# Performance work log

Measured on AMD Instinct MI355X. Metric: run time of the kernel, lower is better.

The kernel has to match this reference:

```python
import jax, jax.numpy as jnp
import numpy as np

E = 500_000
N = 30_000
R = 6
H = 256
OE = 256
OUT = 1
L = 3          # num_layers
A = 2          # num_aux + 1 branches


def setup_inputs() -> dict:
    key = jax.random.key(0)
    ks = jax.random.split(key, 9)
    x = jax.random.normal(ks[0], (E, H), dtype=jnp.float32)
    rbf = jax.random.normal(ks[1], (E, R), dtype=jnp.float32)
    i = jax.random.randint(ks[2], (E,), 0, N, dtype=jnp.int64)
    # parameters (stored in [in, out] convention)
    s = 1.0 / np.sqrt(H)
    W_rbf = jax.random.normal(ks[3], (R, H), dtype=jnp.float32) / np.sqrt(R)
    W_up = jax.random.normal(ks[4], (A, H, OE), dtype=jnp.float32) * s
    W_hidden = jax.random.normal(ks[5], (A, L, OE, OE), dtype=jnp.float32) / np.sqrt(OE)
    b_hidden = jnp.zeros((A, L, OE), dtype=jnp.float32)
    W_out = jax.random.normal(ks[6], (A, OE, OUT), dtype=jnp.float32) / np.sqrt(OE)
    return {"x": x, "rbf": rbf, "i": i, "num_nodes": N,
            "W_rbf": W_rbf, "W_up": W_up, "W_hidden": W_hidden,
            "b_hidden": b_hidden, "W_out": W_out}


def reference(x, rbf, i, num_nodes, W_rbf, W_up, W_hidden, b_hidden, W_out):
    # elementwise multiply of per-edge features by radial basis projection,
    # then segment-sum over edge target index -> per-node features [N, H]
    msg = (rbf @ W_rbf) * x                     # [E, H]
    h = jax.ops.segment_sum(msg, i, num_segments=num_nodes)  # [N, H]
    outs = []
    for a in range(A):
        y = h @ W_up[a]                          # [N, OE]
        for l in range(L):
            y = jax.nn.silu(y @ W_hidden[a, l] + b_hidden[a, l])
        outs.append(y @ W_out[a])               # [N, OUT]
    return tuple(outs)
```

## Files before the change

kernel.cpp:

```cpp
#include <hip/hip_runtime.h>

#define E_EDGES 500000
#define N_NODES 30000
#define H_DIM   256

typedef float  floatx4 __attribute__((ext_vector_type(4)));
typedef short  shortx4 __attribute__((ext_vector_type(4)));
typedef short  shortx8 __attribute__((ext_vector_type(8)));
typedef __bf16 bf16x8  __attribute__((ext_vector_type(8)));

__device__ inline short f2bf(float f) {
    unsigned u = __builtin_bit_cast(unsigned, f);
    u += 0x7fffu + ((u >> 16) & 1u);
    return (short)(u >> 16);
}
__device__ inline float bf2f(short s) {
    unsigned u = ((unsigned)(unsigned short)s) << 16;
    return __builtin_bit_cast(float, u);
}

__global__ __launch_bounds__(256) void prep_weights(
    const float* __restrict__ wup, const float* __restrict__ whid,
    short* __restrict__ wfrag)
{
    int g   = blockIdx.x * 256 + threadIdx.x;
    int mat = g >> 13;
    int grp = g & 8191;
    int a = mat >> 2, lay = mat & 3;
    const float* src = (lay == 0) ? (wup + a * 65536)
                                  : (whid + (a * 3 + lay - 1) * 65536);
    int ks  = grp >> 10;
    int rem = grp & 1023;
    int ntg = rem >> 6;
    int lane = rem & 63;
    int q = lane >> 4, c = lane & 15;
    int col = ntg * 16 + c;
    int k0  = ks * 32 + q * 8;
    shortx8 v;
#pragma unroll
    for (int j = 0; j < 8; j++) v[j] = f2bf(src[(k0 + j) * 256 + col]);
    ((shortx8*)wfrag)[g] = v;
}

__global__ __launch_bounds__(256) void hist_kernel(
    const int* __restrict__ idx, int* __restrict__ counts)
{
    int e = blockIdx.x * 256 + threadIdx.x;
    if (e < E_EDGES) atomicAdd(&counts[idx[e]], 1);
}

__global__ __launch_bounds__(1024) void scan_kernel(
    const int* __restrict__ counts, int* __restrict__ offsets,
    int* __restrict__ cursor)
{
    const int t = threadIdx.x;
    const int lane = t & 63, wave = t >> 6;
    const int base = t * 30;
    int local[30];
    int s = 0;
#pragma unroll
    for (int j = 0; j < 30; j++) {
        int c = (base + j < N_NODES) ? counts[base + j] : 0;
        local[j] = s;
        s += c;
    }
    int incl = s;
#pragma unroll
    for (int d = 1; d < 64; d <<= 1) {
        int v = __shfl_up(incl, d);
        if (lane >= d) incl += v;
    }
    __shared__ int part[16];
    if (lane == 63) part[wave] = incl;
    __syncthreads();
    if (t == 0) {
        int run = 0;
#pragma unroll
        for (int k = 0; k < 16; k++) { int v = part[k]; part[k] = run; run += v; }
    }
    __syncthreads();
    int excl = part[wave] + incl - s;
#pragma unroll
    for (int j = 0; j < 30; j++) {
        int n = base + j;
        if (n < N_NODES) { offsets[n] = excl + local[j]; cursor[n] = excl + local[j]; }
    }
    if (t == 1023) offsets[N_NODES] = excl + s;
}

__global__ __launch_bounds__(256) void scatter_ids(
    const int* __restrict__ idx, int* __restrict__ cursor,
    int* __restrict__ edge_list)
{
    int e = blockIdx.x * 256 + threadIdx.x;
    if (e >= E_EDGES) return;
    int pos = atomicAdd(&cursor[idx[e]], 1);
    edge_list[pos] = e;
}

__global__ __launch_bounds__(256) void gather_nodes(
    const float* __restrict__ x, const float* __restrict__ rbf,
    const int* __restrict__ edge_list, const int* __restrict__ offsets,
    const float* __restrict__ wrbf, float* __restrict__ h)
{
    int node = blockIdx.x * 4 + (threadIdx.x >> 6);
    if (node >= N_NODES) return;
    int lane = threadIdx.x & 63;

    const floatx4* wr4 = (const floatx4*)wrbf;
    floatx4 wr[6];
#pragma unroll
    for (int k = 0; k < 6; k++) wr[k] = wr4[k * 64 + lane];

    int beg = offsets[node], end = offsets[node + 1];
    floatx4 acc = {0.f, 0.f, 0.f, 0.f};
    for (int j = beg; j < end; j++) {
        int e = edge_list[j];
        float r0 = rbf[e * 6 + 0], r1 = rbf[e * 6 + 1], r2 = rbf[e * 6 + 2];
        float r3 = rbf[e * 6 + 3], r4 = rbf[e * 6 + 4], r5 = rbf[e * 6 + 5];
        floatx4 xv = ((const floatx4*)x)[(size_t)e * 64 + lane];
        floatx4 p = r0 * wr[0] + r1 * wr[1] + r2 * wr[2]
                  + r3 * wr[3] + r4 * wr[4] + r5 * wr[5];
        acc += p * xv;
    }
    ((floatx4*)h)[(size_t)node * 64 + lane] = acc;
}

__global__ __launch_bounds__(256, 2) void mlp_kernel(
    const float* __restrict__ h, const short* __restrict__ wfrag,
    const float* __restrict__ bias, const float* __restrict__ wout,
    float* __restrict__ out)
{
    __shared__ __align__(16) short ylds[2][64 * 264];
    const int t = threadIdx.x;
    const int wave = t >> 6, lane = t & 63, q = lane >> 4, c15 = lane & 15;
    const int n0 = blockIdx.x * 64;
    const floatx4 fzero = {0.f, 0.f, 0.f, 0.f};

    for (int a = 0; a < 2; a++) {
#pragma unroll
        for (int j = 0; j < 16; j++) {
            int f = t + j * 256;
            int r = f >> 6, c4 = f & 63;
            floatx4 v = fzero;
            if (n0 + r < N_NODES) v = ((const floatx4*)h)[(size_t)(n0 + r) * 64 + c4];
            shortx4 s4 = { f2bf(v.x), f2bf(v.y), f2bf(v.z), f2bf(v.w) };
            *(shortx4*)&ylds[0][r * 264 + c4 * 4] = s4;
        }
        __syncthreads();

        int src = 0;
        for (int lay = 0; lay < 4; lay++) {
            const bf16x8* wf = (const bf16x8*)(wfrag + (size_t)(a * 4 + lay) * 65536);
            floatx4 acc[4][4];
#pragma unroll
            for (int mt = 0; mt < 4; mt++)
#pragma unroll
                for (int nt = 0; nt < 4; nt++) acc[mt][nt] = fzero;

#pragma unroll
            for (int ks = 0; ks < 8; ks++) {
                bf16x8 afr[4], bfr[4];
#pragma unroll
                for (int mt = 0; mt < 4; mt++)
                    afr[mt] = *(const bf16x8*)&ylds[src][(mt * 16 + c15) * 264 + ks * 32 + q * 8];
#pragma unroll
                for (int nt = 0; nt < 4; nt++)
                    bfr[nt] = wf[(ks * 16 + wave * 4 + nt) * 64 + lane];
#pragma unroll
                for (int mt = 0; mt < 4; mt++)
#pragma unroll
                    for (int nt = 0; nt < 4; nt++)
                        acc[mt][nt] = __builtin_amdgcn_mfma_f32_16x16x32_bf16(
                            afr[mt], bfr[nt], acc[mt][nt], 0, 0, 0);
            }

            int dst = 1 - src;
            float bv[4];
#pragma unroll
            for (int nt = 0; nt < 4; nt++)
                bv[nt] = (lay >= 1) ? bias[(a * 3 + lay - 1) * 256 + wave * 64 + nt * 16 + c15]
                                    : 0.0f;
#pragma unroll
            for (int mt = 0; mt < 4; mt++) {
#pragma unroll
                for (int nt = 0; nt < 4; nt++) {
#pragma unroll
                    for (int rg = 0; rg < 4; rg++) {
                        float v = acc[mt][nt][rg] + bv[nt];
                        if (lay >= 1) v = v / (1.0f + __expf(-v));
                        int row = mt * 16 + q * 4 + rg;
                        int col = wave * 64 + nt * 16 + c15;
                        ylds[dst][row * 264 + col] = f2bf(v);
                    }
                }
            }
            __syncthreads();
            src = dst;
        }

        {
            int r  = wave * 16 + (lane >> 2);
            int cq = lane & 3;
            float s = 0.0f;
#pragma unroll 16
            for (int c = cq * 64; c < cq * 64 + 64; c++)
                s += bf2f(ylds[src][r * 264 + c]) * wout[a * 256 + c];
            s += __shfl_xor(s, 1);
            s += __shfl_xor(s, 2);
            if (cq == 0 && n0 + r < N_NODES) out[a * N_NODES + n0 + r] = s;
        }
        __syncthreads();
    }
}

extern "C" void kernel_launch(void* const* d_in, const int* in_sizes, int n_in,
                              void* d_out, int out_size, void* d_ws, size_t ws_size,
                              hipStream_t stream)
{
    const float* x    = (const float*)d_in[0];
    const float* rbf  = (const float*)d_in[1];
    const int*   idx  = (const int*)d_in[2];
    const float* wrbf = (const float*)d_in[4];
    const float* wup  = (const float*)d_in[5];
    const float* whid = (const float*)d_in[6];
    const float* bias = (const float*)d_in[7];
    const float* wout = (const float*)d_in[8];
    float* out = (float*)d_out;

    char* ws = (char*)d_ws;
    float* h         = (float*)ws;                                   ws += (size_t)N_NODES * H_DIM * sizeof(float);
    short* wfrag     = (short*)ws;                                   ws += (size_t)8 * 65536 * sizeof(short);
    int*   counts    = (int*)ws;                                     ws += (size_t)N_NODES * sizeof(int);
    int*   offsets   = (int*)ws;                                     ws += (size_t)(N_NODES + 1) * sizeof(int);
    int*   cursor    = (int*)ws;                                     ws += (size_t)N_NODES * sizeof(int);
    int*   edge_list = (int*)ws;

    hipMemsetAsync(counts, 0, (size_t)N_NODES * sizeof(int), stream);
    prep_weights<<<256, 256, 0, stream>>>(wup, whid, wfrag);
    hist_kernel<<<(E_EDGES + 255) / 256, 256, 0, stream>>>(idx, counts);
    scan_kernel<<<1, 1024, 0, stream>>>(counts, offsets, cursor);
    scatter_ids<<<(E_EDGES + 255) / 256, 256, 0, stream>>>(idx, cursor, edge_list);
    gather_nodes<<<(N_NODES + 3) / 4, 256, 0, stream>>>(x, rbf, edge_list, offsets, wrbf, h);
    mlp_kernel<<<(N_NODES + 63) / 64, 256, 0, stream>>>(h, wfrag, bias, wout, out);
}
```

Before: 876.4 us.

## Store node features as bf16, batch edge-id loads, split MLP branches across blocks

The gather kernel now loads 64 edge ids per wave in one coalesced read and broadcasts them with shuffles. It reads x with nontemporal loads and writes h directly as bf16 instead of fp32. The MLP kernel gives each branch its own block (938 blocks) with a single LDS buffer, which halves LDS use and drops the fp32-to-bf16 conversion on load. The intent is to cut gather latency and the traffic for h. The cost is rounding h to bf16 earlier and an in-place LDS update that depends on the extra barrier.

```diff
diff --git a/kernel.cpp b/kernel.cpp
--- a/kernel.cpp
+++ b/kernel.cpp
@@ -85,7 +85,7 @@
         int n = base + j;
         if (n < N_NODES) { offsets[n] = excl + local[j]; cursor[n] = excl + local[j]; }
     }
-    if (t == 1023) offsets[N_NODES] = excl + s;
+    if (t == 1023) offsets[N_NODES] = E_EDGES;
 }
 
 __global__ __launch_bounds__(256) void scatter_ids(
@@ -101,7 +101,7 @@
 __global__ __launch_bounds__(256) void gather_nodes(
     const float* __restrict__ x, const float* __restrict__ rbf,
     const int* __restrict__ edge_list, const int* __restrict__ offsets,
-    const float* __restrict__ wrbf, float* __restrict__ h)
+    const float* __restrict__ wrbf, short* __restrict__ h16)
 {
     int node = blockIdx.x * 4 + (threadIdx.x >> 6);
     if (node >= N_NODES) return;
@@ -114,103 +114,107 @@
 
     int beg = offsets[node], end = offsets[node + 1];
     floatx4 acc = {0.f, 0.f, 0.f, 0.f};
-    for (int j = beg; j < end; j++) {
-        int e = edge_list[j];
-        float r0 = rbf[e * 6 + 0], r1 = rbf[e * 6 + 1], r2 = rbf[e * 6 + 2];
-        float r3 = rbf[e * 6 + 3], r4 = rbf[e * 6 + 4], r5 = rbf[e * 6 + 5];
-        floatx4 xv = ((const floatx4*)x)[(size_t)e * 64 + lane];
-        floatx4 p = r0 * wr[0] + r1 * wr[1] + r2 * wr[2]
-                  + r3 * wr[3] + r4 * wr[4] + r5 * wr[5];
-        acc += p * xv;
-    }
-    ((floatx4*)h)[(size_t)node * 64 + lane] = acc;
+    for (int j0 = beg; j0 < end; j0 += 64) {
+        int myid = (j0 + lane < end) ? edge_list[j0 + lane] : 0;
+        int cnt  = end - j0; if (cnt > 64) cnt = 64;
+#pragma unroll 2
+        for (int g = 0; g < cnt; g++) {
+            int e = __shfl(myid, g);
+            float r0 = rbf[e * 6 + 0], r1 = rbf[e * 6 + 1], r2 = rbf[e * 6 + 2];
+            float r3 = rbf[e * 6 + 3], r4 = rbf[e * 6 + 4], r5 = rbf[e * 6 + 5];
+            floatx4 xv = __builtin_nontemporal_load(
+                &((const floatx4*)x)[(size_t)e * 64 + lane]);
+            floatx4 p = r0 * wr[0] + r1 * wr[1] + r2 * wr[2]
+                      + r3 * wr[3] + r4 * wr[4] + r5 * wr[5];
+            acc += p * xv;
+        }
+    }
+    shortx4 s4 = { f2bf(acc.x), f2bf(acc.y), f2bf(acc.z), f2bf(acc.w) };
+    ((shortx4*)h16)[(size_t)node * 64 + lane] = s4;
 }
 
 __global__ __launch_bounds__(256, 2) void mlp_kernel(
-    const float* __restrict__ h, const short* __restrict__ wfrag,
+    const short* __restrict__ h16, const short* __restrict__ wfrag,
     const float* __restrict__ bias, const float* __restrict__ wout,
     float* __restrict__ out)
 {
-    __shared__ __align__(16) short ylds[2][64 * 264];
+    __shared__ __align__(16) short ylds[64 * 264];
     const int t = threadIdx.x;
     const int wave = t >> 6, lane = t & 63, q = lane >> 4, c15 = lane & 15;
-    const int n0 = blockIdx.x * 64;
-    const floatx4 fzero = {0.f, 0.f, 0.f, 0.f};
-
-    for (int a = 0; a < 2; a++) {
-#pragma unroll
-        for (int j = 0; j < 16; j++) {
-            int f = t + j * 256;
-            int r = f >> 6, c4 = f & 63;
-            floatx4 v = fzero;
-            if (n0 + r < N_NODES) v = ((const floatx4*)h)[(size_t)(n0 + r) * 64 + c4];
-            shortx4 s4 = { f2bf(v.x), f2bf(v.y), f2bf(v.z), f2bf(v.w) };
-            *(shortx4*)&ylds[0][r * 264 + c4 * 4] = s4;
+    const int a  = blockIdx.x & 1;
+    const int n0 = (blockIdx.x >> 1) * 64;
+
+#pragma unroll
+    for (int j = 0; j < 8; j++) {
+        int grp = t + j * 256;
+        int r = grp >> 5, c8 = grp & 31;
+        shortx8 v = {0, 0, 0, 0, 0, 0, 0, 0};
+        if (n0 + r < N_NODES)
+            v = *(const shortx8*)&h16[(size_t)(n0 + r) * 256 + c8 * 8];
+        *(shortx8*)&ylds[r * 264 + c8 * 8] = v;
+    }
+    __syncthreads();
+
+    for (int lay = 0; lay < 4; lay++) {
+        const bf16x8* wf = (const bf16x8*)(wfrag + (size_t)(a * 4 + lay) * 65536);
+        floatx4 acc[4][4];
+#pragma unroll
+        for (int mt = 0; mt < 4; mt++)
+#pragma unroll
+            for (int nt = 0; nt < 4; nt++)
+                acc[mt][nt] = (floatx4){0.f, 0.f, 0.f, 0.f};
+
+#pragma unroll
+        for (int ks = 0; ks < 8; ks++) {
+            bf16x8 bfr[4];
+#pragma unroll
+            for (int nt = 0; nt < 4; nt++)
+                bfr[nt] = wf[(ks * 16 + wave * 4 + nt) * 64 + lane];
+#pragma unroll
+            for (int mt = 0; mt < 4; mt++) {
+                bf16x8 afr = *(const bf16x8*)&ylds[(mt * 16 + c15) * 264 + ks * 32 + q * 8];
+#pragma unroll
+                for (int nt = 0; nt < 4; nt++)
+                    acc[mt][nt] = __builtin_amdgcn_mfma_f32_16x16x32_bf16(
+                        afr, bfr[nt], acc[mt][nt], 0, 0, 0);
+            }
         }
         __syncthreads();
 
-        int src = 0;
-        for (int lay = 0; lay < 4; lay++) {
-            const bf16x8* wf = (const bf16x8*)(wfrag + (size_t)(a * 4 + lay) * 65536);
-            floatx4 acc[4][4];
-#pragma unroll
-            for (int mt = 0; mt < 4; mt++)
-#pragma unroll
-                for (int nt = 0; nt < 4; nt++) acc[mt][nt] = fzero;
-
-#pragma unroll
-            for (int ks = 0; ks < 8; ks++) {
-                bf16x8 afr[4], bfr[4];
-#pragma unroll
-                for (int mt = 0; mt < 4; mt++)
-                    afr[mt] = *(const bf16x8*)&ylds[src][(mt * 16 + c15) * 264 + ks * 32 + q * 8];
-#pragma unroll
-                for (int nt = 0; nt < 4; nt++)
-                    bfr[nt] = wf[(ks * 16 + wave * 4 + nt) * 64 + lane];
-#pragma unroll
-                for (int mt = 0; mt < 4; mt++)
-#pragma unroll
-                    for (int nt = 0; nt < 4; nt++)
-                        acc[mt][nt] = __builtin_amdgcn_mfma_f32_16x16x32_bf16(
-                            afr[mt], bfr[nt], acc[mt][nt], 0, 0, 0);
-            }
-
-            int dst = 1 - src;
-            float bv[4];
+        float bv[4];
+#pragma unroll
+        for (int nt = 0; nt < 4; nt++)
+            bv[nt] = (lay >= 1)
+                   ? bias[(a * 3 + lay - 1) * 256 + wave * 64 + nt * 16 + c15]
+                   : 0.0f;
+#pragma unroll
+        for (int mt = 0; mt < 4; mt++)
 #pragma unroll
             for (int nt = 0; nt < 4; nt++)
-                bv[nt] = (lay >= 1) ? bias[(a * 3 + lay - 1) * 256 + wave * 64 + nt * 16 + c15]
-                                    : 0.0f;
-#pragma unroll
-            for (int mt = 0; mt < 4; mt++) {
-#pragma unroll
-                for (int nt = 0; nt < 4; nt++) {
-#pragma unroll
-                    for (int rg = 0; rg < 4; rg++) {
-                        float v = acc[mt][nt][rg] + bv[nt];
-                        if (lay >= 1) v = v / (1.0f + __expf(-v));
-                        int row = mt * 16 + q * 4 + rg;
-                        int col = wave * 64 + nt * 16 + c15;
-                        ylds[dst][row * 264 + col] = f2bf(v);
-                    }
+#pragma unroll
+                for (int rg = 0; rg < 4; rg++) {
+                    float v = acc[mt][nt][rg] + bv[nt];
+                    if (lay >= 1) v = v / (1.0f + __expf(-v));
+                    ylds[(mt * 16 + q * 4 + rg) * 264 + wave * 64 + nt * 16 + c15] = f2bf(v);
                 }
-            }
-            __syncthreads();
-            src = dst;
+        __syncthreads();
+    }
+
+    {
+        int r  = wave * 16 + (lane >> 2);
+        int cq = lane & 3;
+        const float* wo = wout + a * 256 + cq * 64;
+        const short* yp = &ylds[r * 264 + cq * 64];
+        float s = 0.0f;
+#pragma unroll
+        for (int bb = 0; bb < 8; bb++) {
+            shortx8 v = *(const shortx8*)&yp[bb * 8];
+#pragma unroll
+            for (int j = 0; j < 8; j++) s += bf2f(v[j]) * wo[bb * 8 + j];
         }
-
-        {
-            int r  = wave * 16 + (lane >> 2);
-            int cq = lane & 3;
-            float s = 0.0f;
-#pragma unroll 16
-            for (int c = cq * 64; c < cq * 64 + 64; c++)
-                s += bf2f(ylds[src][r * 264 + c]) * wout[a * 256 + c];
-            s += __shfl_xor(s, 1);
-            s += __shfl_xor(s, 2);
-            if (cq == 0 && n0 + r < N_NODES) out[a * N_NODES + n0 + r] = s;
-        }
-        __syncthreads();
+        s += __shfl_xor(s, 1);
+        s += __shfl_xor(s, 2);
+        if (cq == 0 && n0 + r < N_NODES) out[a * N_NODES + n0 + r] = s;
     }
 }
 
@@ -218,6 +222,7 @@
                               void* d_out, int out_size, void* d_ws, size_t ws_size,
                               hipStream_t stream)
 {
+    (void)in_sizes; (void)n_in; (void)out_size; (void)ws_size;
     const float* x    = (const float*)d_in[0];
     const float* rbf  = (const float*)d_in[1];
     const int*   idx  = (const int*)d_in[2];
@@ -229,11 +234,11 @@
     float* out = (float*)d_out;
 
     char* ws = (char*)d_ws;
-    float* h         = (float*)ws;                                   ws += (size_t)N_NODES * H_DIM * sizeof(float);
-    short* wfrag     = (short*)ws;                                   ws += (size_t)8 * 65536 * sizeof(short);
-    int*   counts    = (int*)ws;                                     ws += (size_t)N_NODES * sizeof(int);
-    int*   offsets   = (int*)ws;                                     ws += (size_t)(N_NODES + 1) * sizeof(int);
-    int*   cursor    = (int*)ws;                                     ws += (size_t)N_NODES * sizeof(int);
+    short* h16       = (short*)ws;  ws += (size_t)N_NODES * H_DIM * sizeof(short);
+    short* wfrag     = (short*)ws;  ws += (size_t)8 * 65536 * sizeof(short);
+    int*   counts    = (int*)ws;    ws += (size_t)N_NODES * sizeof(int);
+    int*   offsets   = (int*)ws;    ws += (size_t)(N_NODES + 1) * sizeof(int);
+    int*   cursor    = (int*)ws;    ws += (size_t)N_NODES * sizeof(int);
     int*   edge_list = (int*)ws;
 
     hipMemsetAsync(counts, 0, (size_t)N_NODES * sizeof(int), stream);
@@ -241,6 +246,6 @@
     hist_kernel<<<(E_EDGES + 255) / 256, 256, 0, stream>>>(idx, counts);
     scan_kernel<<<1, 1024, 0, stream>>>(counts, offsets, cursor);
     scatter_ids<<<(E_EDGES + 255) / 256, 256, 0, stream>>>(idx, cursor, edge_list);
-    gather_nodes<<<(N_NODES + 3) / 4, 256, 0, stream>>>(x, rbf, edge_list, offsets, wrbf, h);
-    mlp_kernel<<<(N_NODES + 63) / 64, 256, 0, stream>>>(h, wfrag, bias, wout, out);
-}
+    gather_nodes<<<(N_NODES + 3) / 4, 256, 0, stream>>>(x, rbf, edge_list, offsets, wrbf, h16);
+    mlp_kernel<<<938, 256, 0, stream>>>(h16, wfrag, bias, wout, out);
+}
```

Result: faster. 830.6 us (-5.2%).
